# Kernel optimization log

Hardware: AMD Instinct MI355X
Metric: run time of the kernel (lower is better)

## Reference

```python
import jax, jax.numpy as jnp
import numpy as np

B, S, E, C, T = 1024, 128, 256, 256, 12


def setup_inputs() -> dict:
    key = jax.random.key(0)
    k1, k2, k3, k4 = jax.random.split(key, 4)
    z_aug2 = jax.random.normal(k1, (B, S, E), dtype=jnp.float32)
    c = jax.random.normal(k2, (B, S, C), dtype=jnp.float32)
    Wk_w = jax.random.normal(k3, (T, E, C), dtype=jnp.float32) * 0.05  # stacked Linear weights
    Wk_b = jax.random.normal(k4, (T, E), dtype=jnp.float32) * 0.05    # stacked Linear biases
    return {"z_aug2": z_aug2, "c": c, "Wk_w": Wk_w, "Wk_b": Wk_b, "t_samples": 50}


def reference(z_aug2, c, Wk_w, Wk_b, t_samples):
    # z_aug2: [B, S, E]; c: [B, S, C]; Wk_w: [T, E, C]; Wk_b: [T, E]; t_samples: python int
    T = Wk_w.shape[0]
    batch = z_aug2.shape[0]
    # encode_samples[i-1] = z_aug2[:, t+i, :] for i in 1..T  -> [T, B, E]
    enc = jnp.transpose(z_aug2[:, t_samples + 1 : t_samples + 1 + T, :], (1, 0, 2))
    # c_t = c[:, :t+1, :]; c_t[:, -1, :] == c[:, t, :]
    c_last = c[:, t_samples, :]  # [B, C]
    # pred[i] = Wk[i](c_last) -> [T, B, E]
    pred = jnp.einsum('bc,tec->tbe', c_last, Wk_w) + Wk_b[:, None, :]
    # total_i = enc[i] @ pred[i].T -> batched [T, B, B]
    scores = jnp.einsum('tbe,tce->tbc', enc, pred)
    # nn.LogSoftmax() on a 2D tensor defaults to dim=1 (over pred index)
    logsm = jax.nn.log_softmax(scores, axis=-1)
    nce = jnp.sum(jnp.diagonal(logsm, axis1=1, axis2=2))
    return -nce / (batch * T)
```

## Files before the change

kernel.cpp:

```cpp
#include <hip/hip_runtime.h>
#include <hip/hip_bf16.h>

constexpr int B = 1024, S = 128, E = 256, C = 256, T = 12;

typedef short s8v __attribute__((ext_vector_type(8)));
typedef float f4v __attribute__((ext_vector_type(4)));

__device__ __forceinline__ short f2bf(float f) {
    unsigned u = __builtin_bit_cast(unsigned, f);
    return (short)((u + 0x7FFFu + ((u >> 16) & 1u)) >> 16);
}
__device__ __forceinline__ s8v cvt8(float4 a, float4 b) {
    s8v o;
    o[0] = f2bf(a.x); o[1] = f2bf(a.y); o[2] = f2bf(a.z); o[3] = f2bf(a.w);
    o[4] = f2bf(b.x); o[5] = f2bf(b.y); o[6] = f2bf(b.z); o[7] = f2bf(b.w);
    return o;
}

__global__ __launch_bounds__(256) void cast_kernel(
    const float* __restrict__ z, const float* __restrict__ c,
    const int* __restrict__ tsp,
    short* __restrict__ enc, short* __restrict__ cl)
{
    const int ts = tsp[0];
    const int N1 = T * B * E;
    int i8 = (blockIdx.x * 256 + threadIdx.x) * 8;
    const float4* src;
    short* dst;
    if (i8 < N1) {
        int t = i8 >> 18;
        int rem = i8 & (B * E - 1);
        int b = rem >> 8, e = rem & (E - 1);
        src = reinterpret_cast<const float4*>(z + (size_t)b * S * E + (size_t)(ts + 1 + t) * E + e);
        dst = enc + i8;
    } else {
        int i2 = i8 - N1;
        int b = i2 >> 8, cc = i2 & (C - 1);
        src = reinterpret_cast<const float4*>(c + (size_t)b * S * C + (size_t)ts * C + cc);
        dst = cl + i2;
    }
    *reinterpret_cast<s8v*>(dst) = cvt8(src[0], src[1]);
}

__global__ __launch_bounds__(512, 2) void pred_kernel(
    const short* __restrict__ cl, const float* __restrict__ wkw,
    short* __restrict__ pred)
{
    int wgid = blockIdx.x;
    int xcd = wgid & 7, q = wgid >> 3;
    int pr = xcd * 3 + (q >> 3);
    int bb = q & 7;
    int t = pr >> 1, eb = pr & 1;

    __shared__ __align__(16) short AS[128 * 256];
    __shared__ __align__(16) short BS[128 * 256];
    const int tid = threadIdx.x;

    #pragma unroll
    for (int it = 0; it < 8; ++it) {
        int idx = it * 512 + tid;
        int r = idx >> 5, s = idx & 31;
        s8v va = *reinterpret_cast<const s8v*>(cl + (size_t)(bb * 128 + r) * 256 + s * 8);
        *reinterpret_cast<s8v*>(AS + r * 256 + ((s ^ (r & 7)) * 8)) = va;
        const float4* pb = reinterpret_cast<const float4*>(
            wkw + ((size_t)t * E + eb * 128 + r) * 256 + s * 8);
        *reinterpret_cast<s8v*>(BS + r * 256 + ((s ^ (r & 7)) * 8)) = cvt8(pb[0], pb[1]);
    }
    __syncthreads();

    const int wv = tid >> 6, ln = tid & 63;
    const int wr = wv >> 2, wc = wv & 3;
    const int lr = ln & 15, lg = ln >> 4;
    f4v acc[4][2] = {};

    #pragma unroll
    for (int kk = 0; kk < 8; ++kk) {
        int slot = kk * 4 + lg;
        s8v a[4], b[2];
        #pragma unroll
        for (int m = 0; m < 4; ++m) {
            int r = wr * 64 + m * 16 + lr;
            a[m] = *reinterpret_cast<const s8v*>(AS + r * 256 + ((slot ^ (r & 7)) * 8));
        }
        #pragma unroll
        for (int n = 0; n < 2; ++n) {
            int r = wc * 32 + n * 16 + lr;
            b[n] = *reinterpret_cast<const s8v*>(BS + r * 256 + ((slot ^ (r & 7)) * 8));
        }
        #pragma unroll
        for (int m = 0; m < 4; ++m)
            #pragma unroll
            for (int n = 0; n < 2; ++n)
                acc[m][n] = __builtin_amdgcn_mfma_f32_16x16x32_bf16(a[m], b[n], acc[m][n], 0, 0, 0);
    }

    #pragma unroll
    for (int m = 0; m < 4; ++m)
        #pragma unroll
        for (int n = 0; n < 2; ++n)
            #pragma unroll
            for (int i = 0; i < 4; ++i) {
                int bg = bb * 128 + wr * 64 + m * 16 + lg * 4 + i;
                int eg = eb * 128 + wc * 32 + n * 16 + lr;
                pred[(size_t)t * B * E + (size_t)bg * E + eg] = f2bf(acc[m][n][i]);
            }
}

__global__ __launch_bounds__(512, 4) void score_kernel(
    const short* __restrict__ enc, const short* __restrict__ pred,
    float* __restrict__ part_m, float* __restrict__ part_s,
    float* __restrict__ diag_g)
{
    int wgid = blockIdx.x;
    int xcd = wgid & 7, q = wgid >> 3;
    int pairid = xcd * 6 + (q >> 4);
    int rb = q & 15;
    int t = pairid >> 2, ci = pairid & 3;

    __shared__ __align__(16) char SM[65536];
    short* encS = reinterpret_cast<short*>(SM);
    short* buf0 = reinterpret_cast<short*>(SM + 32768);
    short* buf1 = reinterpret_cast<short*>(SM + 49152);
    float* pm = reinterpret_cast<float*>(SM + 32768);
    float* ps = pm + 256;

    const int tid = threadIdx.x;
    const short* enc_t = enc + (size_t)t * B * E;
    const short* pred_t = pred + (size_t)t * B * E;

    const int h0 = tid, h1 = tid + 512;
    const int col0 = h0 >> 2, sl0 = h0 & 3;
    const int col1 = h1 >> 2, sl1 = h1 & 3;
    const short* g0 = pred_t + (size_t)(ci * 256 + col0) * 256 + sl0 * 8;
    const short* g1 = pred_t + (size_t)(ci * 256 + col1) * 256 + sl1 * 8;
    const int l0 = sl0 * 2048 + col0 * 8;
    const int l1 = sl1 * 2048 + col1 * 8;

    s8v R0 = *reinterpret_cast<const s8v*>(g0);
    s8v R1 = *reinterpret_cast<const s8v*>(g1);
    #pragma unroll
    for (int it = 0; it < 4; ++it) {
        int idx = it * 512 + tid;
        int r = idx >> 5, s = idx & 31;
        s8v v = *reinterpret_cast<const s8v*>(enc_t + (size_t)(rb * 64 + r) * 256 + s * 8);
        *reinterpret_cast<s8v*>(encS + r * 256 + ((s ^ (r & 7)) * 8)) = v;
    }
    *reinterpret_cast<s8v*>(buf0 + l0) = R0;
    *reinterpret_cast<s8v*>(buf0 + l1) = R1;
    R0 = *reinterpret_cast<const s8v*>(g0 + 32);
    R1 = *reinterpret_cast<const s8v*>(g1 + 32);
    __syncthreads();

    const int wv = tid >> 6, ln = tid & 63;
    const int wr = wv >> 2, wc = wv & 3;
    const int lr = ln & 15, lg = ln >> 4;
    f4v acc[4][2] = {};

    #pragma unroll
    for (int ke = 0; ke < 8; ++ke) {
        short* cur = (ke & 1) ? buf1 : buf0;
        short* nxt = (ke & 1) ? buf0 : buf1;
        if (ke < 7) {
            *reinterpret_cast<s8v*>(nxt + l0) = R0;
            *reinterpret_cast<s8v*>(nxt + l1) = R1;
        }
        if (ke < 6) {
            R0 = *reinterpret_cast<const s8v*>(g0 + (ke + 2) * 32);
            R1 = *reinterpret_cast<const s8v*>(g1 + (ke + 2) * 32);
        }
        s8v p[4], e[2];
        #pragma unroll
        for (int a = 0; a < 4; ++a)
            p[a] = *reinterpret_cast<const s8v*>(cur + lg * 2048 + (wc * 64 + a * 16 + lr) * 8);
        #pragma unroll
        for (int b = 0; b < 2; ++b) {
            int er = wr * 32 + b * 16 + lr;
            int sf = ke * 4 + lg;
            e[b] = *reinterpret_cast<const s8v*>(encS + er * 256 + ((sf ^ (er & 7)) * 8));
        }
        #pragma unroll
        for (int a = 0; a < 4; ++a)
            #pragma unroll
            for (int b = 0; b < 2; ++b)
                acc[a][b] = __builtin_amdgcn_mfma_f32_16x16x32_bf16(p[a], e[b], acc[a][b], 0, 0, 0);
        __syncthreads();
    }

    #pragma unroll
    for (int b = 0; b < 2; ++b) {
        float mx = -1e30f;
        #pragma unroll
        for (int a = 0; a < 4; ++a)
            #pragma unroll
            for (int i = 0; i < 4; ++i) mx = fmaxf(mx, acc[a][b][i]);
        mx = fmaxf(mx, __shfl_xor(mx, 16));
        mx = fmaxf(mx, __shfl_xor(mx, 32));
        float sm = 0.0f;
        #pragma unroll
        for (int a = 0; a < 4; ++a)
            #pragma unroll
            for (int i = 0; i < 4; ++i) sm += __expf(acc[a][b][i] - mx);
        sm += __shfl_xor(sm, 16);
        sm += __shfl_xor(sm, 32);
        if (lg == 0) {
            pm[wc * 64 + wr * 32 + b * 16 + lr] = mx;
            ps[wc * 64 + wr * 32 + b * 16 + lr] = sm;
        }
        int rg = rb * 64 + wr * 32 + b * 16 + lr;
        if ((rg >> 8) == ci) {
            int dl = rg & 255;
            if ((dl >> 6) == wc && ((dl >> 2) & 3) == lg) {
                float dv = 0.0f;
                #pragma unroll
                for (int a = 0; a < 4; ++a)
                    #pragma unroll
                    for (int i = 0; i < 4; ++i)
                        if (((dl >> 4) & 3) == a && (dl & 3) == i) dv = acc[a][b][i];
                diag_g[t * B + rg] = dv;
            }
        }
    }
    __syncthreads();
    if (tid < 64) {
        float M = pm[tid];
        #pragma unroll
        for (int w = 1; w < 4; ++w) M = fmaxf(M, pm[w * 64 + tid]);
        float Ss = 0.0f;
        #pragma unroll
        for (int w = 0; w < 4; ++w) Ss += ps[w * 64 + tid] * __expf(pm[w * 64 + tid] - M);
        size_t o = (size_t)ci * (T * B) + (size_t)t * B + rb * 64 + tid;
        part_m[o] = M;
        part_s[o] = Ss;
    }
}

__global__ __launch_bounds__(1024) void combine_kernel(
    const float* __restrict__ part_m, const float* __restrict__ part_s,
    const float* __restrict__ diag_g, float* __restrict__ bs)
{
    int row = blockIdx.x * 1024 + threadIdx.x;
    float m0 = part_m[row],             m1 = part_m[T * B + row];
    float m2 = part_m[2 * T * B + row], m3 = part_m[3 * T * B + row];
    float s0 = part_s[row],             s1 = part_s[T * B + row];
    float s2 = part_s[2 * T * B + row], s3 = part_s[3 * T * B + row];
    float M = fmaxf(fmaxf(m0, m1), fmaxf(m2, m3));
    float Ss = s0 * __expf(m0 - M) + s1 * __expf(m1 - M)
             + s2 * __expf(m2 - M) + s3 * __expf(m3 - M);
    float val = diag_g[row] - (M + logf(Ss));

    for (int o = 1; o < 64; o <<= 1) val += __shfl_xor(val, o);
    __shared__ float red[16];
    int wv = threadIdx.x >> 6, lnn = threadIdx.x & 63;
    if (lnn == 0) red[wv] = val;
    __syncthreads();
    if (threadIdx.x == 0) {
        float tot = 0.0f;
        #pragma unroll
        for (int w = 0; w < 16; ++w) tot += red[w];
        bs[blockIdx.x] = tot;
    }
}

__global__ void final_kernel(const float* __restrict__ bs, float* __restrict__ out)
{
    float s = (threadIdx.x < 12) ? bs[threadIdx.x] : 0.0f;
    for (int o = 1; o < 16; o <<= 1) s += __shfl_xor(s, o);
    if (threadIdx.x == 0) out[0] = -s / (float)(B * T);
}

extern "C" void kernel_launch(void* const* d_in, const int* in_sizes, int n_in,
                              void* d_out, int out_size, void* d_ws, size_t ws_size,
                              hipStream_t stream)
{
    (void)in_sizes; (void)n_in; (void)out_size; (void)ws_size;
    const float* z   = (const float*)d_in[0];
    const float* c   = (const float*)d_in[1];
    const float* wkw = (const float*)d_in[2];
    const int*   tsp = (const int*)d_in[4];

    char* w = (char*)d_ws;
    short* enc    = (short*)(w);
    short* pred   = (short*)(w + 6291456);
    short* cl     = (short*)(w + 12582912);
    float* part_m = (float*)(w + 13107200);
    float* part_s = (float*)(w + 13303808);
    float* diag_g = (float*)(w + 13500416);
    float* bs     = (float*)(w + 13549568);

    cast_kernel<<<1664, 256, 0, stream>>>(z, c, tsp, enc, cl);
    pred_kernel<<<192, 512, 0, stream>>>(cl, wkw, pred);
    score_kernel<<<768, 512, 0, stream>>>(enc, pred, part_m, part_s, diag_g);
    combine_kernel<<<12, 1024, 0, stream>>>(part_m, part_s, diag_g, bs);
    final_kernel<<<1, 64, 0, stream>>>(bs, (float*)d_out);
}
```

Before: 35.13 us.

## Fuse casts into GEMMs and fold softmax combine into score kernel via online softmax

Removes the separate cast kernel by converting c and z to bf16 directly when loading into shared memory in the pred and score kernels. The score kernel now has each workgroup sweep all four column chunks with a running online log-sum-exp, keeping the diagonal in LDS. It accumulates the final loss with an atomicAdd, which eliminates the combine and final kernels and the partial buffers. This cuts the launch count from five to two, but shrinks the score grid from 768 to 192 workgroups, each doing four times the work with less parallelism. It also relies on float atomic ordering and on pred_kernel zeroing the output before score_kernel runs.

```diff
diff --git a/kernel.cpp b/kernel.cpp
--- a/kernel.cpp
+++ b/kernel.cpp
@@ -17,40 +17,17 @@
     return o;
 }
 
-__global__ __launch_bounds__(256) void cast_kernel(
-    const float* __restrict__ z, const float* __restrict__ c,
-    const int* __restrict__ tsp,
-    short* __restrict__ enc, short* __restrict__ cl)
-{
-    const int ts = tsp[0];
-    const int N1 = T * B * E;
-    int i8 = (blockIdx.x * 256 + threadIdx.x) * 8;
-    const float4* src;
-    short* dst;
-    if (i8 < N1) {
-        int t = i8 >> 18;
-        int rem = i8 & (B * E - 1);
-        int b = rem >> 8, e = rem & (E - 1);
-        src = reinterpret_cast<const float4*>(z + (size_t)b * S * E + (size_t)(ts + 1 + t) * E + e);
-        dst = enc + i8;
-    } else {
-        int i2 = i8 - N1;
-        int b = i2 >> 8, cc = i2 & (C - 1);
-        src = reinterpret_cast<const float4*>(c + (size_t)b * S * C + (size_t)ts * C + cc);
-        dst = cl + i2;
-    }
-    *reinterpret_cast<s8v*>(dst) = cvt8(src[0], src[1]);
-}
-
-__global__ __launch_bounds__(512, 2) void pred_kernel(
-    const short* __restrict__ cl, const float* __restrict__ wkw,
-    short* __restrict__ pred)
+__global__ __launch_bounds__(512) void pred_kernel(
+    const float* __restrict__ c, const float* __restrict__ wkw,
+    const int* __restrict__ tsp, short* __restrict__ pred, float* __restrict__ out)
 {
     int wgid = blockIdx.x;
     int xcd = wgid & 7, q = wgid >> 3;
     int pr = xcd * 3 + (q >> 3);
     int bb = q & 7;
     int t = pr >> 1, eb = pr & 1;
+    if (wgid == 0 && threadIdx.x == 0) out[0] = 0.0f;
+    const int ts = tsp[0];
 
     __shared__ __align__(16) short AS[128 * 256];
     __shared__ __align__(16) short BS[128 * 256];
@@ -60,8 +37,9 @@
     for (int it = 0; it < 8; ++it) {
         int idx = it * 512 + tid;
         int r = idx >> 5, s = idx & 31;
-        s8v va = *reinterpret_cast<const s8v*>(cl + (size_t)(bb * 128 + r) * 256 + s * 8);
-        *reinterpret_cast<s8v*>(AS + r * 256 + ((s ^ (r & 7)) * 8)) = va;
+        const float4* pa = reinterpret_cast<const float4*>(
+            c + (size_t)(bb * 128 + r) * S * C + (size_t)ts * C + s * 8);
+        *reinterpret_cast<s8v*>(AS + r * 256 + ((s ^ (r & 7)) * 8)) = cvt8(pa[0], pa[1]);
         const float4* pb = reinterpret_cast<const float4*>(
             wkw + ((size_t)t * E + eb * 128 + r) * 256 + s * 8);
         *reinterpret_cast<s8v*>(BS + r * 256 + ((s ^ (r & 7)) * 8)) = cvt8(pb[0], pb[1]);
@@ -106,121 +84,143 @@
             }
 }
 
-__global__ __launch_bounds__(512, 4) void score_kernel(
-    const short* __restrict__ enc, const short* __restrict__ pred,
-    float* __restrict__ part_m, float* __restrict__ part_s,
-    float* __restrict__ diag_g)
+__global__ __launch_bounds__(512) void score_kernel(
+    const float* __restrict__ z, const short* __restrict__ pred,
+    const int* __restrict__ tsp, float* __restrict__ out)
 {
-    int wgid = blockIdx.x;
-    int xcd = wgid & 7, q = wgid >> 3;
-    int pairid = xcd * 6 + (q >> 4);
-    int rb = q & 15;
-    int t = pairid >> 2, ci = pairid & 3;
+    const int wgid = blockIdx.x;
+    const int t = wgid >> 4, rb = wgid & 15;
+    const int ts = tsp[0];
 
     __shared__ __align__(16) char SM[65536];
     short* encS = reinterpret_cast<short*>(SM);
     short* buf0 = reinterpret_cast<short*>(SM + 32768);
     short* buf1 = reinterpret_cast<short*>(SM + 49152);
-    float* pm = reinterpret_cast<float*>(SM + 32768);
-    float* ps = pm + 256;
+    float* pm    = reinterpret_cast<float*>(SM + 32768);
+    float* ps    = pm + 256;
+    float* diagS = ps + 256;
 
     const int tid = threadIdx.x;
-    const short* enc_t = enc + (size_t)t * B * E;
     const short* pred_t = pred + (size_t)t * B * E;
 
-    const int h0 = tid, h1 = tid + 512;
-    const int col0 = h0 >> 2, sl0 = h0 & 3;
-    const int col1 = h1 >> 2, sl1 = h1 & 3;
-    const short* g0 = pred_t + (size_t)(ci * 256 + col0) * 256 + sl0 * 8;
-    const short* g1 = pred_t + (size_t)(ci * 256 + col1) * 256 + sl1 * 8;
+    const int col0 = tid >> 2,          sl0 = tid & 3;
+    const int col1 = (tid + 512) >> 2,  sl1 = tid & 3;
+    const short* base0 = pred_t + (size_t)col0 * 256 + sl0 * 8;
+    const short* base1 = pred_t + (size_t)col1 * 256 + sl1 * 8;
     const int l0 = sl0 * 2048 + col0 * 8;
     const int l1 = sl1 * 2048 + col1 * 8;
 
-    s8v R0 = *reinterpret_cast<const s8v*>(g0);
-    s8v R1 = *reinterpret_cast<const s8v*>(g1);
+    s8v R0 = *reinterpret_cast<const s8v*>(base0);
+    s8v R1 = *reinterpret_cast<const s8v*>(base1);
     #pragma unroll
     for (int it = 0; it < 4; ++it) {
         int idx = it * 512 + tid;
         int r = idx >> 5, s = idx & 31;
-        s8v v = *reinterpret_cast<const s8v*>(enc_t + (size_t)(rb * 64 + r) * 256 + s * 8);
-        *reinterpret_cast<s8v*>(encS + r * 256 + ((s ^ (r & 7)) * 8)) = v;
+        const float4* pz = reinterpret_cast<const float4*>(
+            z + (size_t)(rb * 64 + r) * S * E + (size_t)(ts + 1 + t) * E + s * 8);
+        *reinterpret_cast<s8v*>(encS + r * 256 + ((s ^ (r & 7)) * 8)) = cvt8(pz[0], pz[1]);
     }
     *reinterpret_cast<s8v*>(buf0 + l0) = R0;
     *reinterpret_cast<s8v*>(buf0 + l1) = R1;
-    R0 = *reinterpret_cast<const s8v*>(g0 + 32);
-    R1 = *reinterpret_cast<const s8v*>(g1 + 32);
+    R0 = *reinterpret_cast<const s8v*>(base0 + 32);
+    R1 = *reinterpret_cast<const s8v*>(base1 + 32);
     __syncthreads();
 
     const int wv = tid >> 6, ln = tid & 63;
     const int wr = wv >> 2, wc = wv & 3;
     const int lr = ln & 15, lg = ln >> 4;
     f4v acc[4][2] = {};
-
-    #pragma unroll
-    for (int ke = 0; ke < 8; ++ke) {
-        short* cur = (ke & 1) ? buf1 : buf0;
-        short* nxt = (ke & 1) ? buf0 : buf1;
-        if (ke < 7) {
-            *reinterpret_cast<s8v*>(nxt + l0) = R0;
-            *reinterpret_cast<s8v*>(nxt + l1) = R1;
+    float m_run[2] = {-1e30f, -1e30f};
+    float s_run[2] = {0.0f, 0.0f};
+    float dreg[2] = {0.0f, 0.0f};
+    int downer[2] = {0, 0};
+
+    #pragma unroll
+    for (int ci = 0; ci < 4; ++ci) {
+        #pragma unroll
+        for (int ke = 0; ke < 8; ++ke) {
+            const int Eix = ci * 8 + ke;
+            short* cur = (Eix & 1) ? buf1 : buf0;
+            short* nxt = (Eix & 1) ? buf0 : buf1;
+            if (Eix < 31) {
+                *reinterpret_cast<s8v*>(nxt + l0) = R0;
+                *reinterpret_cast<s8v*>(nxt + l1) = R1;
+            }
+            if (Eix < 30) {
+                const int E2 = Eix + 2;
+                const int off = (E2 >> 3) * 65536 + (E2 & 7) * 32;
+                R0 = *reinterpret_cast<const s8v*>(base0 + off);
+                R1 = *reinterpret_cast<const s8v*>(base1 + off);
+            }
+            s8v p[4], e[2];
+            #pragma unroll
+            for (int a = 0; a < 4; ++a)
+                p[a] = *reinterpret_cast<const s8v*>(cur + lg * 2048 + (wc * 64 + a * 16 + lr) * 8);
+            #pragma unroll
+            for (int b = 0; b < 2; ++b) {
+                int er = wr * 32 + b * 16 + lr;
+                int sf = ke * 4 + lg;
+                e[b] = *reinterpret_cast<const s8v*>(encS + er * 256 + ((sf ^ (er & 7)) * 8));
+            }
+            #pragma unroll
+            for (int a = 0; a < 4; ++a)
+                #pragma unroll
+                for (int b = 0; b < 2; ++b)
+                    acc[a][b] = __builtin_amdgcn_mfma_f32_16x16x32_bf16(p[a], e[b], acc[a][b], 0, 0, 0);
+
+            if (ke == 7) {
+                #pragma unroll
+                for (int b = 0; b < 2; ++b) {
+                    float mx = -1e30f;
+                    #pragma unroll
+                    for (int a = 0; a < 4; ++a)
+                        #pragma unroll
+                        for (int i = 0; i < 4; ++i) mx = fmaxf(mx, acc[a][b][i]);
+                    mx = fmaxf(mx, __shfl_xor(mx, 16));
+                    mx = fmaxf(mx, __shfl_xor(mx, 32));
+                    float sm = 0.0f;
+                    #pragma unroll
+                    for (int a = 0; a < 4; ++a)
+                        #pragma unroll
+                        for (int i = 0; i < 4; ++i) sm += __expf(acc[a][b][i] - mx);
+                    sm += __shfl_xor(sm, 16);
+                    sm += __shfl_xor(sm, 32);
+
+                    int rg = rb * 64 + wr * 32 + b * 16 + lr;
+                    if ((rg >> 8) == ci) {
+                        int dl = rg & 255;
+                        if ((dl >> 6) == wc && ((dl >> 2) & 3) == lg) {
+                            #pragma unroll
+                            for (int a = 0; a < 4; ++a)
+                                #pragma unroll
+                                for (int i = 0; i < 4; ++i)
+                                    if (((dl >> 4) & 3) == a && (dl & 3) == i) dreg[b] = acc[a][b][i];
+                            downer[b] = 1;
+                        }
+                    }
+                    float mn = fmaxf(m_run[b], mx);
+                    s_run[b] = s_run[b] * __expf(m_run[b] - mn) + sm * __expf(mx - mn);
+                    m_run[b] = mn;
+                    #pragma unroll
+                    for (int a = 0; a < 4; ++a)
+                        #pragma unroll
+                        for (int i = 0; i < 4; ++i) acc[a][b][i] = 0.0f;
+                }
+            }
+            __syncthreads();
         }
-        if (ke < 6) {
-            R0 = *reinterpret_cast<const s8v*>(g0 + (ke + 2) * 32);
-            R1 = *reinterpret_cast<const s8v*>(g1 + (ke + 2) * 32);
-        }
-        s8v p[4], e[2];
-        #pragma unroll
-        for (int a = 0; a < 4; ++a)
-            p[a] = *reinterpret_cast<const s8v*>(cur + lg * 2048 + (wc * 64 + a * 16 + lr) * 8);
-        #pragma unroll
-        for (int b = 0; b < 2; ++b) {
-            int er = wr * 32 + b * 16 + lr;
-            int sf = ke * 4 + lg;
-            e[b] = *reinterpret_cast<const s8v*>(encS + er * 256 + ((sf ^ (er & 7)) * 8));
-        }
-        #pragma unroll
-        for (int a = 0; a < 4; ++a)
-            #pragma unroll
-            for (int b = 0; b < 2; ++b)
-                acc[a][b] = __builtin_amdgcn_mfma_f32_16x16x32_bf16(p[a], e[b], acc[a][b], 0, 0, 0);
-        __syncthreads();
-    }
-
-    #pragma unroll
-    for (int b = 0; b < 2; ++b) {
-        float mx = -1e30f;
-        #pragma unroll
-        for (int a = 0; a < 4; ++a)
-            #pragma unroll
-            for (int i = 0; i < 4; ++i) mx = fmaxf(mx, acc[a][b][i]);
-        mx = fmaxf(mx, __shfl_xor(mx, 16));
-        mx = fmaxf(mx, __shfl_xor(mx, 32));
-        float sm = 0.0f;
-        #pragma unroll
-        for (int a = 0; a < 4; ++a)
-            #pragma unroll
-            for (int i = 0; i < 4; ++i) sm += __expf(acc[a][b][i] - mx);
-        sm += __shfl_xor(sm, 16);
-        sm += __shfl_xor(sm, 32);
-        if (lg == 0) {
-            pm[wc * 64 + wr * 32 + b * 16 + lr] = mx;
-            ps[wc * 64 + wr * 32 + b * 16 + lr] = sm;
-        }
-        int rg = rb * 64 + wr * 32 + b * 16 + lr;
-        if ((rg >> 8) == ci) {
-            int dl = rg & 255;
-            if ((dl >> 6) == wc && ((dl >> 2) & 3) == lg) {
-                float dv = 0.0f;
-                #pragma unroll
-                for (int a = 0; a < 4; ++a)
-                    #pragma unroll
-                    for (int i = 0; i < 4; ++i)
-                        if (((dl >> 4) & 3) == a && (dl & 3) == i) dv = acc[a][b][i];
-                diag_g[t * B + rg] = dv;
-            }
-        }
-    }
+    }
+
+    if (lg == 0) {
+        pm[wc * 64 + wr * 32 + lr]      = m_run[0];
+        ps[wc * 64 + wr * 32 + lr]      = s_run[0];
+        pm[wc * 64 + wr * 32 + 16 + lr] = m_run[1];
+        ps[wc * 64 + wr * 32 + 16 + lr] = s_run[1];
+    }
+    if (downer[0]) diagS[wr * 32 + lr]      = dreg[0];
+    if (downer[1]) diagS[wr * 32 + 16 + lr] = dreg[1];
     __syncthreads();
+
     if (tid < 64) {
         float M = pm[tid];
         #pragma unroll
@@ -228,44 +228,11 @@
         float Ss = 0.0f;
         #pragma unroll
         for (int w = 0; w < 4; ++w) Ss += ps[w * 64 + tid] * __expf(pm[w * 64 + tid] - M);
-        size_t o = (size_t)ci * (T * B) + (size_t)t * B + rb * 64 + tid;
-        part_m[o] = M;
-        part_s[o] = Ss;
-    }
-}
-
-__global__ __launch_bounds__(1024) void combine_kernel(
-    const float* __restrict__ part_m, const float* __restrict__ part_s,
-    const float* __restrict__ diag_g, float* __restrict__ bs)
-{
-    int row = blockIdx.x * 1024 + threadIdx.x;
-    float m0 = part_m[row],             m1 = part_m[T * B + row];
-    float m2 = part_m[2 * T * B + row], m3 = part_m[3 * T * B + row];
-    float s0 = part_s[row],             s1 = part_s[T * B + row];
-    float s2 = part_s[2 * T * B + row], s3 = part_s[3 * T * B + row];
-    float M = fmaxf(fmaxf(m0, m1), fmaxf(m2, m3));
-    float Ss = s0 * __expf(m0 - M) + s1 * __expf(m1 - M)
-             + s2 * __expf(m2 - M) + s3 * __expf(m3 - M);
-    float val = diag_g[row] - (M + logf(Ss));
-
-    for (int o = 1; o < 64; o <<= 1) val += __shfl_xor(val, o);
-    __shared__ float red[16];
-    int wv = threadIdx.x >> 6, lnn = threadIdx.x & 63;
-    if (lnn == 0) red[wv] = val;
-    __syncthreads();
-    if (threadIdx.x == 0) {
-        float tot = 0.0f;
-        #pragma unroll
-        for (int w = 0; w < 16; ++w) tot += red[w];
-        bs[blockIdx.x] = tot;
-    }
-}
-
-__global__ void final_kernel(const float* __restrict__ bs, float* __restrict__ out)
-{
-    float s = (threadIdx.x < 12) ? bs[threadIdx.x] : 0.0f;
-    for (int o = 1; o < 16; o <<= 1) s += __shfl_xor(s, o);
-    if (threadIdx.x == 0) out[0] = -s / (float)(B * T);
+        float val = diagS[tid] - (M + logf(Ss));
+        #pragma unroll
+        for (int o = 1; o < 64; o <<= 1) val += __shfl_xor(val, o);
+        if (tid == 0) atomicAdd(out, -val / (float)(B * T));
+    }
 }
 
 extern "C" void kernel_launch(void* const* d_in, const int* in_sizes, int n_in,
@@ -278,18 +245,8 @@
     const float* wkw = (const float*)d_in[2];
     const int*   tsp = (const int*)d_in[4];
 
-    char* w = (char*)d_ws;
-    short* enc    = (short*)(w);
-    short* pred   = (short*)(w + 6291456);
-    short* cl     = (short*)(w + 12582912);
-    float* part_m = (float*)(w + 13107200);
-    float* part_s = (float*)(w + 13303808);
-    float* diag_g = (float*)(w + 13500416);
-    float* bs     = (float*)(w + 13549568);
-
-    cast_kernel<<<1664, 256, 0, stream>>>(z, c, tsp, enc, cl);
-    pred_kernel<<<192, 512, 0, stream>>>(cl, wkw, pred);
-    score_kernel<<<768, 512, 0, stream>>>(enc, pred, part_m, part_s, diag_g);
-    combine_kernel<<<12, 1024, 0, stream>>>(part_m, part_s, diag_g, bs);
-    final_kernel<<<1, 64, 0, stream>>>(bs, (float*)d_out);
-}
+    short* pred = (short*)d_ws;
+
+    pred_kernel<<<192, 512, 0, stream>>>(c, wkw, tsp, pred, (float*)d_out);
+    score_kernel<<<192, 512, 0, stream>>>(z, pred, tsp, (float*)d_out);
+}
```

Measured after the change: 37.72 us. 7.3% more time.
